# Performance work log

Hardware: AMD Instinct MI355X
Metric: run time of the kernel (lower is better)

## Reference

```python
import jax, jax.numpy as jnp
import numpy as np

N_NODES = 100000
N_EDGES = 600000
IN_FEAT = 128
HID = 128
N_CLASSES = 64


def setup_inputs() -> dict:
    key = jax.random.key(0)
    ks = jax.random.split(key, 24)
    inp = {}
    inp["x"] = jax.random.normal(ks[0], (N_NODES, IN_FEAT), dtype=jnp.float32)
    for i, r in enumerate(["r0", "r1"]):
        inp[f"src_{r}"] = jax.random.randint(ks[1 + 3 * i], (N_EDGES,), 0, N_NODES, dtype=jnp.int32)
        inp[f"dst_{r}"] = jax.random.randint(ks[2 + 3 * i], (N_EDGES,), 0, N_NODES, dtype=jnp.int32)
        inp[f"ew_{r}"] = jax.random.uniform(ks[3 + 3 * i], (N_EDGES,), dtype=jnp.float32)
    def glorot(k, shape):
        fan = (shape[0] + shape[1]) / 2.0
        return jax.random.normal(k, shape, dtype=jnp.float32) / jnp.sqrt(fan)
    j = 7
    for r in ["r0", "r1"]:
        inp[f"Ws0_{r}"] = glorot(ks[j], (IN_FEAT, HID)); j += 1
        inp[f"Wn0_{r}"] = glorot(ks[j], (IN_FEAT, HID)); j += 1
        inp[f"b0_{r}"] = jnp.zeros((HID,), jnp.float32)
        inp[f"Wp_{r}"] = glorot(ks[j], (HID, HID)); j += 1
        inp[f"bp_{r}"] = jnp.zeros((HID,), jnp.float32)
        inp[f"Ws1_{r}"] = glorot(ks[j], (HID, N_CLASSES)); j += 1
        inp[f"Wn1_{r}"] = glorot(ks[j], (HID, N_CLASSES)); j += 1
        inp[f"b1_{r}"] = jnp.zeros((N_CLASSES,), jnp.float32)
    return inp


def _mean_agg(feat, src, dst, ew, n_nodes):
    # edge-weighted messages, mean over in-edges (divide by in-degree as DGL does)
    msg = feat[src] * ew[:, None]                      # [E, d]
    s = jax.ops.segment_sum(msg, dst, num_segments=n_nodes)
    deg = jax.ops.segment_sum(jnp.ones_like(ew), dst, num_segments=n_nodes)
    return s / jnp.maximum(deg, 1.0)[:, None]


def _max_agg(feat, src, dst, ew, n_nodes):
    msg = feat[src] * ew[:, None]                      # [E, d]
    m = jax.ops.segment_max(msg, dst, num_segments=n_nodes)
    deg = jax.ops.segment_sum(jnp.ones_like(ew), dst, num_segments=n_nodes)
    return jnp.where(deg[:, None] > 0, m, 0.0)         # zero for isolated nodes


def reference(x, src_r0, dst_r0, ew_r0, src_r1, dst_r1, ew_r1,
              Ws0_r0, Wn0_r0, b0_r0, Ws0_r1, Wn0_r1, b0_r1,
              Wp_r0, bp_r0, Ws1_r0, Wn1_r0, b1_r0,
              Wp_r1, bp_r1, Ws1_r1, Wn1_r1, b1_r1):
    n = x.shape[0]
    # Layer 0: per-relation SAGEConv(mean), HeteroGraphConv aggregate='sum', then relu
    h = jnp.zeros((n, Wn0_r0.shape[1]), x.dtype)
    for src, dst, ew, Ws, Wn, b in [
        (src_r0, dst_r0, ew_r0, Ws0_r0, Wn0_r0, b0_r0),
        (src_r1, dst_r1, ew_r1, Ws0_r1, Wn0_r1, b0_r1),
    ]:
        agg = _mean_agg(x, src, dst, ew, n)
        h = h + x @ Ws + agg @ Wn + b
    h = jax.nn.relu(h)
    # Classifier layer: per-relation SAGEConv(pool): relu(fc_pool(h_src)) -> max-agg
    logits = jnp.zeros((n, Wn1_r0.shape[1]), x.dtype)
    for src, dst, ew, Wp, bp, Ws, Wn, b in [
        (src_r0, dst_r0, ew_r0, Wp_r0, bp_r0, Ws1_r0, Wn1_r0, b1_r0),
        (src_r1, dst_r1, ew_r1, Wp_r1, bp_r1, Ws1_r1, Wn1_r1, b1_r1),
    ]:
        hp = jax.nn.relu(h @ Wp + bp)
        agg = _max_agg(hp, src, dst, ew, n)
        logits = logits + h @ Ws + agg @ Wn + b
    return logits
```

## Files before the change

### kernel.cpp

```cpp
#include <hip/hip_runtime.h>

typedef short bf16x8 __attribute__((ext_vector_type(8)));
typedef float f32x4 __attribute__((ext_vector_type(4)));
typedef unsigned short u16;
typedef unsigned int u32;

#define NN 100000
#define NE 600000
#define PART 12500
#define ECH 4688

__device__ __forceinline__ u16 f2b(float f) {
    u32 u = __float_as_uint(f);
    return (u16)((u + 0x7FFFu + ((u >> 16) & 1u)) >> 16);
}

__global__ void fused_setup(
    const float* __restrict__ x, u16* __restrict__ xo,
    const float* __restrict__ Ws0_0, const float* __restrict__ Ws0_1,
    const float* __restrict__ Wn0_0, const float* __restrict__ Wn0_1,
    const float* __restrict__ Wp_0,  const float* __restrict__ Wp_1,
    const float* __restrict__ Ws1_0, const float* __restrict__ Ws1_1,
    const float* __restrict__ Wn1_0, const float* __restrict__ Wn1_1,
    const float* __restrict__ b0_0, const float* __restrict__ b0_1,
    const float* __restrict__ b1_0, const float* __restrict__ b1_1,
    const float* __restrict__ bp_0, const float* __restrict__ bp_1,
    u16* __restrict__ w, float* __restrict__ bsum0, float* __restrict__ bsum1,
    float* __restrict__ bpc)
{
    int bb = blockIdx.x;
    if (bb < 12500) {
        int t = bb * 256 + threadIdx.x;
        const float4 v = reinterpret_cast<const float4*>(x)[t];
        ushort4 r; r.x = f2b(v.x); r.y = f2b(v.y); r.z = f2b(v.z); r.w = f2b(v.w);
        reinterpret_cast<ushort4*>(xo)[t] = r;
    } else {
        int t = (bb - 12500) * 256 + threadIdx.x;
        if (t < 81920) {
            int m = t >> 14, u = t & 16383;
            int n = u >> 7, k = u & 127;
            float v;
            if (m == 0)      v = Ws0_0[k * 128 + n] + Ws0_1[k * 128 + n];
            else if (m == 1) v = Wn0_0[k * 128 + n];
            else if (m == 2) v = Wn0_1[k * 128 + n];
            else if (m == 3) v = Wp_0[k * 128 + n];
            else             v = Wp_1[k * 128 + n];
            w[t] = f2b(v);
        } else if (t < 106496) {
            int u = t - 81920;
            int m = u >> 13; u &= 8191;
            int n = u >> 7, k = u & 127;
            float v;
            if (m == 0)      v = Ws1_0[k * 64 + n] + Ws1_1[k * 64 + n];
            else if (m == 1) v = Wn1_0[k * 64 + n];
            else             v = Wn1_1[k * 64 + n];
            w[t] = f2b(v);
        } else if (t < 106624) {
            int i = t - 106496; bsum0[i] = b0_0[i] + b0_1[i];
        } else if (t < 106688) {
            int i = t - 106624; bsum1[i] = b1_0[i] + b1_1[i];
        } else if (t < 106944) {
            int i = t - 106688; bpc[i] = (i < 128) ? bp_0[i] : bp_1[i - 128];
        }
    }
}

__global__ __launch_bounds__(256) void deg_part(
    const int* __restrict__ d0, const int* __restrict__ d1,
    int* __restrict__ g0, int* __restrict__ g1)
{
    int part = blockIdx.x & 7;
    int sub = blockIdx.x >> 3;
    int rel = sub & 1;
    int chunk = sub >> 1;
    const int lo = part * PART, hi = lo + PART;
    const int* d = rel ? d1 : d0;
    int* g = rel ? g1 : g0;
    const int e0 = chunk * ECH;
    const int e1 = min(e0 + ECH, NE);
    for (int e = e0 + threadIdx.x; e < e1; e += 256) {
        int dd = d[e];
        if (dd >= lo && dd < hi) atomicAdd(&g[dd], 1);
    }
}

__global__ void scan_local(const int* __restrict__ deg0, const int* __restrict__ deg1,
                           int* __restrict__ offs0, int* __restrict__ offs1,
                           int* __restrict__ bsA, int* __restrict__ bsB)
{
    __shared__ int sm[1024];
    int rel = blockIdx.x >= 98;
    int blk = blockIdx.x - rel * 98;
    const int* in = rel ? deg1 : deg0;
    int* out = rel ? offs1 : offs0;
    int* bsum = rel ? bsB : bsA;
    int t = threadIdx.x;
    int i = blk * 1024 + t;
    int v = (i < NN) ? in[i] : 0;
    sm[t] = v;
    __syncthreads();
    for (int off = 1; off < 1024; off <<= 1) {
        int add = (t >= off) ? sm[t - off] : 0;
        __syncthreads();
        sm[t] += add;
        __syncthreads();
    }
    if (i < NN) out[i] = sm[t] - v;
    if (t == 1023) bsum[blk] = sm[1023];
}

__global__ void scan_bsums(int* __restrict__ bsA, int* __restrict__ bsB)
{
    __shared__ int sm[128];
    int* bsum = blockIdx.x ? bsB : bsA;
    int t = threadIdx.x;
    int v = (t < 98) ? bsum[t] : 0;
    sm[t] = v;
    __syncthreads();
    for (int off = 1; off < 128; off <<= 1) {
        int add = (t >= off) ? sm[t - off] : 0;
        __syncthreads();
        sm[t] += add;
        __syncthreads();
    }
    if (t < 98) bsum[t] = sm[t] - v;
}

__global__ void scan_add(int* __restrict__ offs0, int* __restrict__ offs1,
                         const int* __restrict__ bsA, const int* __restrict__ bsB,
                         int* __restrict__ cur0, int* __restrict__ cur1,
                         u32* __restrict__ csr0, u32* __restrict__ csr1)
{
    int rel = blockIdx.x >= 392;
    int i = (blockIdx.x - rel * 392) * 256 + threadIdx.x;
    int* offs = rel ? offs1 : offs0;
    int* cur = rel ? cur1 : cur0;
    const int* bsum = rel ? bsB : bsA;
    if (i < NN) {
        int v = offs[i] + bsum[i >> 10];
        offs[i] = v;
        cur[i] = v;
    }
    if (i == 0) offs[NN] = NE;
    if (blockIdx.x == 0 && threadIdx.x < 8) {
        csr0[NE + threadIdx.x] = 0;
        csr1[NE + threadIdx.x] = 0;
    }
}

__global__ __launch_bounds__(256) void build_csr_part(
    const int* __restrict__ src0, const int* __restrict__ dst0,
    const float* __restrict__ ew0,
    const int* __restrict__ src1, const int* __restrict__ dst1,
    const float* __restrict__ ew1,
    int* __restrict__ cur0, int* __restrict__ cur1,
    u32* __restrict__ csr0, u32* __restrict__ csr1)
{
    int part = blockIdx.x & 7;
    int sub = blockIdx.x >> 3;
    int rel = sub & 1;
    int chunk = sub >> 1;
    const int lo = part * PART, hi = lo + PART;
    const int* src = rel ? src1 : src0;
    const int* dst = rel ? dst1 : dst0;
    const float* ew = rel ? ew1 : ew0;
    int* cur = rel ? cur1 : cur0;
    u32* csr = rel ? csr1 : csr0;
    const int e0 = chunk * ECH;
    const int e1 = min(e0 + ECH, NE);
    for (int e = e0 + threadIdx.x; e < e1; e += 256) {
        int d = dst[e];
        if (d >= lo && d < hi) {
            int p = atomicAdd(&cur[d], 1);
            u32 q = (__float_as_uint(ew[e]) + 0x10000u) >> 17;
            csr[p] = ((u32)src[e] << 15) | q;
        }
    }
}

template<bool MAXAGG>
__global__ __launch_bounds__(256) void gather(
    const u16* __restrict__ F0, const u16* __restrict__ F1,
    const int* __restrict__ offs0, const u32* __restrict__ csr0, u16* __restrict__ o0,
    const int* __restrict__ offs1, const u32* __restrict__ csr1, u16* __restrict__ o1)
{
    int b = blockIdx.x;
    int rel = b >= 25000;
    const u16* F = rel ? F1 : F0;
    const int* offs = rel ? offs1 : offs0;
    const u32* csr = rel ? csr1 : csr0;
    u16* out = rel ? o1 : o0;
    int node = (b - rel * 25000) * 4 + (threadIdx.x >> 6);
    int lane = threadIdx.x & 63;
    int beg = __builtin_amdgcn_readfirstlane(offs[node]);
    int end = __builtin_amdgcn_readfirstlane(offs[node + 1]);
    const int lane2 = lane << 1;

    float acc0[8], acc1[8];
#pragma unroll
    for (int i = 0; i < 8; ++i) { acc0[i] = 0.f; acc1[i] = 0.f; }

    for (int e = beg; e < end; e += 8) {
        u32 E[8];
#pragma unroll
        for (int i = 0; i < 8; ++i)
            E[i] = __builtin_amdgcn_readfirstlane(csr[e + i]);
        float wq[8];
        wq[0] = __uint_as_float(E[0] << 17);
#pragma unroll
        for (int i = 1; i < 8; ++i)
            wq[i] = (e + i < end) ? __uint_as_float(E[i] << 17) : 0.f;
        u32 v[8];
#pragma unroll
        for (int i = 0; i < 8; ++i)
            v[i] = *reinterpret_cast<const u32*>(F + ((size_t)(E[i] >> 15) << 7) + lane2);
#pragma unroll
        for (int i = 0; i < 8; ++i) {
            float f0 = __uint_as_float(v[i] << 16);
            float f1 = __uint_as_float(v[i] & 0xFFFF0000u);
            if (MAXAGG) {
                acc0[i] = fmaxf(acc0[i], f0 * wq[i]);
                acc1[i] = fmaxf(acc1[i], f1 * wq[i]);
            } else {
                acc0[i] = fmaf(f0, wq[i], acc0[i]);
                acc1[i] = fmaf(f1, wq[i], acc1[i]);
            }
        }
    }

    float a0, a1, scale;
    if (MAXAGG) {
        a0 = fmaxf(fmaxf(fmaxf(acc0[0], acc0[1]), fmaxf(acc0[2], acc0[3])),
                   fmaxf(fmaxf(acc0[4], acc0[5]), fmaxf(acc0[6], acc0[7])));
        a1 = fmaxf(fmaxf(fmaxf(acc1[0], acc1[1]), fmaxf(acc1[2], acc1[3])),
                   fmaxf(fmaxf(acc1[4], acc1[5]), fmaxf(acc1[6], acc1[7])));
        scale = 1.f;
    } else {
        a0 = ((acc0[0] + acc0[1]) + (acc0[2] + acc0[3])) +
             ((acc0[4] + acc0[5]) + (acc0[6] + acc0[7]));
        a1 = ((acc1[0] + acc1[1]) + (acc1[2] + acc1[3])) +
             ((acc1[4] + acc1[5]) + (acc1[6] + acc1[7]));
        scale = 1.f / fmaxf((float)(end - beg), 1.f);
    }
    ushort2 r; r.x = f2b(a0 * scale); r.y = f2b(a1 * scale);
    *reinterpret_cast<ushort2*>(out + (size_t)node * 128 + lane2) = r;
}

template<int NPAIR, int COLGROUPS, int WAVES, bool RELU, bool OUTF32, bool DUAL>
__global__ __launch_bounds__(WAVES * 64, 2) void gemm_reg(
    const u16* __restrict__ A0, const u16* __restrict__ A1, const u16* __restrict__ A2,
    const u16* __restrict__ BT, const float* __restrict__ bias,
    float* __restrict__ outF, u16* __restrict__ outB, u16* __restrict__ outB2)
{
    constexpr int NC = COLGROUPS * 32;
    constexpr int RT = WAVES / COLGROUPS;
    constexpr int OST = DUAL ? (NC / 2) : NC;
    constexpr int NTILES = NN / 32;
    const int w = threadIdx.x >> 6, l = threadIdx.x & 63;
    const int cg = w % COLGROUPS, rsub = w / COLGROUPS;
    const int l15 = l & 15, lk = (l >> 4) << 3, rq = (l >> 4) << 2;

    bf16x8 bfr[NPAIR][4][2];
#pragma unroll
    for (int p = 0; p < NPAIR; ++p)
#pragma unroll
        for (int ks = 0; ks < 4; ++ks)
#pragma unroll
            for (int cf = 0; cf < 2; ++cf) {
                int n = p * NC + cg * 32 + cf * 16 + l15;
                bfr[p][ks][cf] = *reinterpret_cast<const bf16x8*>(BT + (size_t)n * 128 + ks * 32 + lk);
            }

    const u16* As[3] = {A0, A1, A2};
    const float bv0 = bias[cg * 32 + l15];
    const float bv1 = bias[cg * 32 + 16 + l15];

    for (int tile = blockIdx.x * RT + rsub; tile < NTILES; tile += gridDim.x * RT) {
        const size_t rowbase = (size_t)tile * 32;

        bf16x8 af[NPAIR][4][2];
#pragma unroll
        for (int p = 0; p < NPAIR; ++p) {
            const u16* A = As[p] + rowbase * 128;
#pragma unroll
            for (int ks = 0; ks < 4; ++ks) {
                const int k0 = ks * 32 + lk;
                af[p][ks][0] = *reinterpret_cast<const bf16x8*>(A + (size_t)l15 * 128 + k0);
                af[p][ks][1] = *reinterpret_cast<const bf16x8*>(A + (size_t)(16 + l15) * 128 + k0);
            }
        }

        f32x4 acc[2][2];
#pragma unroll
        for (int rf = 0; rf < 2; ++rf)
#pragma unroll
            for (int cf = 0; cf < 2; ++cf)
                acc[rf][cf] = f32x4{0.f, 0.f, 0.f, 0.f};

#pragma unroll
        for (int p = 0; p < NPAIR; ++p)
#pragma unroll
            for (int ks = 0; ks < 4; ++ks) {
                acc[0][0] = __builtin_amdgcn_mfma_f32_16x16x32_bf16(af[p][ks][0], bfr[p][ks][0], acc[0][0], 0, 0, 0);
                acc[0][1] = __builtin_amdgcn_mfma_f32_16x16x32_bf16(af[p][ks][0], bfr[p][ks][1], acc[0][1], 0, 0, 0);
                acc[1][0] = __builtin_amdgcn_mfma_f32_16x16x32_bf16(af[p][ks][1], bfr[p][ks][0], acc[1][0], 0, 0, 0);
                acc[1][1] = __builtin_amdgcn_mfma_f32_16x16x32_bf16(af[p][ks][1], bfr[p][ks][1], acc[1][1], 0, 0, 0);
            }

        u16* ob = outB;
        if (DUAL && cg >= 4) ob = outB2;
        const int colbase = (DUAL ? (cg & 3) : cg) * 32;
#pragma unroll
        for (int cf = 0; cf < 2; ++cf) {
            const int col = colbase + cf * 16 + l15;
            const float bv = cf ? bv1 : bv0;
#pragma unroll
            for (int rf = 0; rf < 2; ++rf) {
#pragma unroll
                for (int j = 0; j < 4; ++j) {
                    const size_t row = rowbase + rf * 16 + rq + j;
                    float v = acc[rf][cf][j] + bv;
                    if (RELU) v = fmaxf(v, 0.f);
                    if (OUTF32) outF[row * OST + col] = v;
                    else        ob[row * OST + col] = f2b(v);
                }
            }
        }
    }
}

extern "C" void kernel_launch(void* const* d_in, const int* in_sizes, int n_in,
                              void* d_out, int out_size, void* d_ws, size_t ws_size,
                              hipStream_t stream)
{
    const float* x     = (const float*)d_in[0];
    const int*   src0  = (const int*)d_in[1];
    const int*   dst0  = (const int*)d_in[2];
    const float* ew0   = (const float*)d_in[3];
    const int*   src1  = (const int*)d_in[4];
    const int*   dst1  = (const int*)d_in[5];
    const float* ew1   = (const float*)d_in[6];
    const float* Ws0_0 = (const float*)d_in[7];
    const float* Wn0_0 = (const float*)d_in[8];
    const float* b0_0  = (const float*)d_in[9];
    const float* Wp_0  = (const float*)d_in[10];
    const float* bp_0  = (const float*)d_in[11];
    const float* Ws1_0 = (const float*)d_in[12];
    const float* Wn1_0 = (const float*)d_in[13];
    const float* b1_0  = (const float*)d_in[14];
    const float* Ws0_1 = (const float*)d_in[15];
    const float* Wn0_1 = (const float*)d_in[16];
    const float* b0_1  = (const float*)d_in[17];
    const float* Wp_1  = (const float*)d_in[18];
    const float* bp_1  = (const float*)d_in[19];
    const float* Ws1_1 = (const float*)d_in[20];
    const float* Wn1_1 = (const float*)d_in[21];
    const float* b1_1  = (const float*)d_in[22];

    char* ws = (char*)d_ws;
    u16*   x16   = (u16*)(ws + 0);
    u16*   h16   = (u16*)(ws + 25600000);
    u16*   a0    = (u16*)(ws + 51200000);
    u16*   a1    = (u16*)(ws + 76800000);
    u16*   hp1   = (u16*)(ws + 102400000);
    u32*   csr0  = (u32*)(ws + 128000000);
    u32*   csr1  = (u32*)(ws + 130400032);
    int*   offs0 = (int*)(ws + 132800064);
    int*   offs1 = (int*)(ws + 133200080);
    int*   cur0  = (int*)(ws + 133600096);
    int*   cur1  = (int*)(ws + 134000096);
    int*   deg0  = (int*)(ws + 134400096);
    int*   deg1  = (int*)(ws + 134800096);
    int*   bsA   = (int*)(ws + 135200096);
    int*   bsB   = (int*)(ws + 135200608);
    u16*   wts   = (u16*)(ws + 135201120);
    float* bsum0 = (float*)(ws + 135414112);
    float* bsum1 = (float*)(ws + 135414624);
    float* bpc   = (float*)(ws + 135415136);

    u16* hp0 = x16;

    hipMemsetAsync(deg0, 0, 800000, stream);
    deg_part<<<2048, 256, 0, stream>>>(dst0, dst1, deg0, deg1);
    fused_setup<<<12918, 256, 0, stream>>>(
        x, x16, Ws0_0, Ws0_1, Wn0_0, Wn0_1, Wp_0, Wp_1,
        Ws1_0, Ws1_1, Wn1_0, Wn1_1, b0_0, b0_1, b1_0, b1_1, bp_0, bp_1,
        wts, bsum0, bsum1, bpc);

    scan_local<<<196, 1024, 0, stream>>>(deg0, deg1, offs0, offs1, bsA, bsB);
    scan_bsums<<<2, 128, 0, stream>>>(bsA, bsB);
    scan_add<<<784, 256, 0, stream>>>(offs0, offs1, bsA, bsB, cur0, cur1, csr0, csr1);
    build_csr_part<<<2048, 256, 0, stream>>>(
        src0, dst0, ew0, src1, dst1, ew1, cur0, cur1, csr0, csr1);

    gather<false><<<50000, 256, 0, stream>>>(x16, x16, offs0, csr0, a0, offs1, csr1, a1);
    gemm_reg<3, 4, 4, true, false, false><<<1024, 256, 0, stream>>>(
        x16, a0, a1, wts, bsum0, nullptr, h16, nullptr);

    gemm_reg<1, 8, 8, true, false, true><<<512, 512, 0, stream>>>(
        h16, nullptr, nullptr, wts + 49152, bpc, nullptr, hp0, hp1);
    gather<true><<<50000, 256, 0, stream>>>(hp0, hp1, offs0, csr0, a0, offs1, csr1, a1);
    gemm_reg<3, 2, 4, false, true, false><<<782, 256, 0, stream>>>(
        h16, a0, a1, wts + 81920, bsum1, (float*)d_out, nullptr, nullptr);
}
```

Baseline: 375.4 us.

## Store node features in 16-column slices so gather blocks hit cache-resident partitions

New measurement: 422.5 us. 1.13x slower.

```diff
diff --git a/kernel.cpp b/kernel.cpp
--- a/kernel.cpp
+++ b/kernel.cpp
@@ -9,6 +9,7 @@
 #define NE 600000
 #define PART 12500
 #define ECH 4688
+#define SL (NN * 16)
 
 __device__ __forceinline__ u16 f2b(float f) {
     u32 u = __float_as_uint(f);
@@ -33,7 +34,9 @@
         int t = bb * 256 + threadIdx.x;
         const float4 v = reinterpret_cast<const float4*>(x)[t];
         ushort4 r; r.x = f2b(v.x); r.y = f2b(v.y); r.z = f2b(v.z); r.w = f2b(v.w);
-        reinterpret_cast<ushort4*>(xo)[t] = r;
+        int node = t >> 5;
+        int fq = (t & 31) << 2;
+        *reinterpret_cast<ushort4*>(xo + (size_t)(fq >> 4) * SL + node * 16 + (fq & 15)) = r;
     } else {
         int t = (bb - 12500) * 256 + threadIdx.x;
         if (t < 81920) {
@@ -128,8 +131,7 @@
 
 __global__ void scan_add(int* __restrict__ offs0, int* __restrict__ offs1,
                          const int* __restrict__ bsA, const int* __restrict__ bsB,
-                         int* __restrict__ cur0, int* __restrict__ cur1,
-                         u32* __restrict__ csr0, u32* __restrict__ csr1)
+                         int* __restrict__ cur0, int* __restrict__ cur1)
 {
     int rel = blockIdx.x >= 392;
     int i = (blockIdx.x - rel * 392) * 256 + threadIdx.x;
@@ -142,10 +144,6 @@
         cur[i] = v;
     }
     if (i == 0) offs[NN] = NE;
-    if (blockIdx.x == 0 && threadIdx.x < 8) {
-        csr0[NE + threadIdx.x] = 0;
-        csr1[NE + threadIdx.x] = 0;
-    }
 }
 
 __global__ __launch_bounds__(256) void build_csr_part(
@@ -178,75 +176,73 @@
     }
 }
 
-template<bool MAXAGG>
-__global__ __launch_bounds__(256) void gather(
-    const u16* __restrict__ F0, const u16* __restrict__ F1,
+template<bool MAXAGG, bool REL2>
+__global__ __launch_bounds__(256) void gather_slice(
+    const u16* __restrict__ Fs,
     const int* __restrict__ offs0, const u32* __restrict__ csr0, u16* __restrict__ o0,
     const int* __restrict__ offs1, const u32* __restrict__ csr1, u16* __restrict__ o1)
 {
-    int b = blockIdx.x;
-    int rel = b >= 25000;
-    const u16* F = rel ? F1 : F0;
-    const int* offs = rel ? offs1 : offs0;
-    const u32* csr = rel ? csr1 : csr0;
-    u16* out = rel ? o1 : o0;
-    int node = (b - rel * 25000) * 4 + (threadIdx.x >> 6);
-    int lane = threadIdx.x & 63;
-    int beg = __builtin_amdgcn_readfirstlane(offs[node]);
-    int end = __builtin_amdgcn_readfirstlane(offs[node + 1]);
-    const int lane2 = lane << 1;
-
-    float acc0[8], acc1[8];
-#pragma unroll
-    for (int i = 0; i < 8; ++i) { acc0[i] = 0.f; acc1[i] = 0.f; }
-
-    for (int e = beg; e < end; e += 8) {
-        u32 E[8];
-#pragma unroll
-        for (int i = 0; i < 8; ++i)
-            E[i] = __builtin_amdgcn_readfirstlane(csr[e + i]);
-        float wq[8];
-        wq[0] = __uint_as_float(E[0] << 17);
-#pragma unroll
-        for (int i = 1; i < 8; ++i)
-            wq[i] = (e + i < end) ? __uint_as_float(E[i] << 17) : 0.f;
-        u32 v[8];
-#pragma unroll
-        for (int i = 0; i < 8; ++i)
-            v[i] = *reinterpret_cast<const u32*>(F + ((size_t)(E[i] >> 15) << 7) + lane2);
-#pragma unroll
-        for (int i = 0; i < 8; ++i) {
-            float f0 = __uint_as_float(v[i] << 16);
-            float f1 = __uint_as_float(v[i] & 0xFFFF0000u);
-            if (MAXAGG) {
-                acc0[i] = fmaxf(acc0[i], f0 * wq[i]);
-                acc1[i] = fmaxf(acc1[i], f1 * wq[i]);
-            } else {
-                acc0[i] = fmaf(f0, wq[i], acc0[i]);
-                acc1[i] = fmaf(f1, wq[i], acc1[i]);
+    const int part = blockIdx.x & 7;
+    int sub = blockIdx.x >> 3;
+    const int* offs = offs0;
+    const u32* csr = csr0;
+    u16* outs = o0;
+    int nper;
+    if (REL2) {
+        int rel = sub & 1; sub >>= 1;
+        if (rel) { offs = offs1; csr = csr1; outs = o1; }
+        nper = 782;
+    } else {
+        nper = 391;
+    }
+    const int l = threadIdx.x & 63;
+    const int wv = threadIdx.x >> 6;
+    const int g = l >> 3, lf = l & 7;
+    const u16* F = Fs + (size_t)part * SL + (lf << 1);
+    u16* out = outs + (size_t)part * SL + (lf << 1);
+
+    const int nbeg = sub * nper;
+    const int nend = min(nbeg + nper, NN);
+    for (int nb = nbeg + (wv << 3); nb < nend; nb += 32) {
+        int node = nb + g;
+        int nc = min(node, NN - 1);
+        int beg = offs[nc];
+        int cnt = (node < nend) ? (offs[nc + 1] - beg) : 0;
+        int last = max(cnt - 1, 0);
+        float a0 = 0.f, a1 = 0.f;
+        for (int base = 0; __any(base < cnt); base += 8) {
+            u32 E[8];
+#pragma unroll
+            for (int j = 0; j < 8; ++j)
+                E[j] = csr[beg + min(base + j, last)];
+            u32 v[8];
+#pragma unroll
+            for (int j = 0; j < 8; ++j)
+                v[j] = *reinterpret_cast<const u32*>(F + ((size_t)(E[j] >> 15) << 4));
+#pragma unroll
+            for (int j = 0; j < 8; ++j) {
+                float wgt = (base + j < cnt) ? __uint_as_float(E[j] << 17) : 0.f;
+                float f0 = __uint_as_float(v[j] << 16);
+                float f1 = __uint_as_float(v[j] & 0xFFFF0000u);
+                if (MAXAGG) {
+                    a0 = fmaxf(a0, f0 * wgt);
+                    a1 = fmaxf(a1, f1 * wgt);
+                } else {
+                    a0 = fmaf(f0, wgt, a0);
+                    a1 = fmaf(f1, wgt, a1);
+                }
             }
         }
-    }
-
-    float a0, a1, scale;
-    if (MAXAGG) {
-        a0 = fmaxf(fmaxf(fmaxf(acc0[0], acc0[1]), fmaxf(acc0[2], acc0[3])),
-                   fmaxf(fmaxf(acc0[4], acc0[5]), fmaxf(acc0[6], acc0[7])));
-        a1 = fmaxf(fmaxf(fmaxf(acc1[0], acc1[1]), fmaxf(acc1[2], acc1[3])),
-                   fmaxf(fmaxf(acc1[4], acc1[5]), fmaxf(acc1[6], acc1[7])));
-        scale = 1.f;
-    } else {
-        a0 = ((acc0[0] + acc0[1]) + (acc0[2] + acc0[3])) +
-             ((acc0[4] + acc0[5]) + (acc0[6] + acc0[7]));
-        a1 = ((acc1[0] + acc1[1]) + (acc1[2] + acc1[3])) +
-             ((acc1[4] + acc1[5]) + (acc1[6] + acc1[7]));
-        scale = 1.f / fmaxf((float)(end - beg), 1.f);
-    }
-    ushort2 r; r.x = f2b(a0 * scale); r.y = f2b(a1 * scale);
-    *reinterpret_cast<ushort2*>(out + (size_t)node * 128 + lane2) = r;
-}
-
-template<int NPAIR, int COLGROUPS, int WAVES, bool RELU, bool OUTF32, bool DUAL>
+        if (node < nend) {
+            float s = MAXAGG ? 1.f : 1.f / fmaxf((float)cnt, 1.f);
+            ushort2 r; r.x = f2b(a0 * s); r.y = f2b(a1 * s);
+            *reinterpret_cast<ushort2*>(out + (size_t)node * 16) = r;
+        }
+    }
+}
+
+template<int NPAIR, int COLGROUPS, int WAVES, bool RELU, bool OUTF32, bool DUAL,
+         int SLICEMASK, bool SLICEC>
 __global__ __launch_bounds__(WAVES * 64, 2) void gemm_reg(
     const u16* __restrict__ A0, const u16* __restrict__ A1, const u16* __restrict__ A2,
     const u16* __restrict__ BT, const float* __restrict__ bias,
@@ -281,12 +277,21 @@
         bf16x8 af[NPAIR][4][2];
 #pragma unroll
         for (int p = 0; p < NPAIR; ++p) {
-            const u16* A = As[p] + rowbase * 128;
+            const u16* A = As[p];
+            const bool sl = (SLICEMASK >> p) & 1;
 #pragma unroll
             for (int ks = 0; ks < 4; ++ks) {
                 const int k0 = ks * 32 + lk;
-                af[p][ks][0] = *reinterpret_cast<const bf16x8*>(A + (size_t)l15 * 128 + k0);
-                af[p][ks][1] = *reinterpret_cast<const bf16x8*>(A + (size_t)(16 + l15) * 128 + k0);
+                size_t off0, off1;
+                if (sl) {
+                    off0 = (size_t)(k0 >> 4) * SL + (rowbase + l15) * 16 + (k0 & 15);
+                    off1 = (size_t)(k0 >> 4) * SL + (rowbase + 16 + l15) * 16 + (k0 & 15);
+                } else {
+                    off0 = (rowbase + l15) * (size_t)128 + k0;
+                    off1 = (rowbase + 16 + l15) * (size_t)128 + k0;
+                }
+                af[p][ks][0] = *reinterpret_cast<const bf16x8*>(A + off0);
+                af[p][ks][1] = *reinterpret_cast<const bf16x8*>(A + off1);
             }
         }
 
@@ -314,6 +319,7 @@
         for (int cf = 0; cf < 2; ++cf) {
             const int col = colbase + cf * 16 + l15;
             const float bv = cf ? bv1 : bv0;
+            const size_t sbase = (size_t)((colbase + cf * 16) >> 4) * SL;
 #pragma unroll
             for (int rf = 0; rf < 2; ++rf) {
 #pragma unroll
@@ -321,8 +327,9 @@
                     const size_t row = rowbase + rf * 16 + rq + j;
                     float v = acc[rf][cf][j] + bv;
                     if (RELU) v = fmaxf(v, 0.f);
-                    if (OUTF32) outF[row * OST + col] = v;
-                    else        ob[row * OST + col] = f2b(v);
+                    if (OUTF32)      outF[row * OST + col] = v;
+                    else if (SLICEC) ob[sbase + row * 16 + l15] = f2b(v);
+                    else             ob[row * OST + col] = f2b(v);
                 }
             }
         }
@@ -358,11 +365,11 @@
     const float* b1_1  = (const float*)d_in[22];
 
     char* ws = (char*)d_ws;
-    u16*   x16   = (u16*)(ws + 0);
+    u16*   x16s  = (u16*)(ws + 0);
     u16*   h16   = (u16*)(ws + 25600000);
-    u16*   a0    = (u16*)(ws + 51200000);
-    u16*   a1    = (u16*)(ws + 76800000);
-    u16*   hp1   = (u16*)(ws + 102400000);
+    u16*   a0s   = (u16*)(ws + 51200000);
+    u16*   a1s   = (u16*)(ws + 76800000);
+    u16*   hp1s  = (u16*)(ws + 102400000);
     u32*   csr0  = (u32*)(ws + 128000000);
     u32*   csr1  = (u32*)(ws + 130400032);
     int*   offs0 = (int*)(ws + 132800064);
@@ -378,28 +385,32 @@
     float* bsum1 = (float*)(ws + 135414624);
     float* bpc   = (float*)(ws + 135415136);
 
-    u16* hp0 = x16;
+    u16* hp0s = x16s;
 
     hipMemsetAsync(deg0, 0, 800000, stream);
     deg_part<<<2048, 256, 0, stream>>>(dst0, dst1, deg0, deg1);
     fused_setup<<<12918, 256, 0, stream>>>(
-        x, x16, Ws0_0, Ws0_1, Wn0_0, Wn0_1, Wp_0, Wp_1,
+        x, x16s, Ws0_0, Ws0_1, Wn0_0, Wn0_1, Wp_0, Wp_1,
         Ws1_0, Ws1_1, Wn1_0, Wn1_1, b0_0, b0_1, b1_0, b1_1, bp_0, bp_1,
         wts, bsum0, bsum1, bpc);
 
     scan_local<<<196, 1024, 0, stream>>>(deg0, deg1, offs0, offs1, bsA, bsB);
     scan_bsums<<<2, 128, 0, stream>>>(bsA, bsB);
-    scan_add<<<784, 256, 0, stream>>>(offs0, offs1, bsA, bsB, cur0, cur1, csr0, csr1);
+    scan_add<<<784, 256, 0, stream>>>(offs0, offs1, bsA, bsB, cur0, cur1);
     build_csr_part<<<2048, 256, 0, stream>>>(
         src0, dst0, ew0, src1, dst1, ew1, cur0, cur1, csr0, csr1);
 
-    gather<false><<<50000, 256, 0, stream>>>(x16, x16, offs0, csr0, a0, offs1, csr1, a1);
-    gemm_reg<3, 4, 4, true, false, false><<<1024, 256, 0, stream>>>(
-        x16, a0, a1, wts, bsum0, nullptr, h16, nullptr);
-
-    gemm_reg<1, 8, 8, true, false, true><<<512, 512, 0, stream>>>(
-        h16, nullptr, nullptr, wts + 49152, bpc, nullptr, hp0, hp1);
-    gather<true><<<50000, 256, 0, stream>>>(hp0, hp1, offs0, csr0, a0, offs1, csr1, a1);
-    gemm_reg<3, 2, 4, false, true, false><<<782, 256, 0, stream>>>(
-        h16, a0, a1, wts + 81920, bsum1, (float*)d_out, nullptr, nullptr);
-}
+    gather_slice<false, true><<<2048, 256, 0, stream>>>(
+        x16s, offs0, csr0, a0s, offs1, csr1, a1s);
+    gemm_reg<3, 4, 4, true, false, false, 0b111, false><<<1024, 256, 0, stream>>>(
+        x16s, a0s, a1s, wts, bsum0, nullptr, h16, nullptr);
+
+    gemm_reg<1, 8, 8, true, false, true, 0, true><<<512, 512, 0, stream>>>(
+        h16, nullptr, nullptr, wts + 49152, bpc, nullptr, hp0s, hp1s);
+    gather_slice<true, false><<<2048, 256, 0, stream>>>(
+        hp0s, offs0, csr0, a0s, nullptr, nullptr, nullptr);
+    gather_slice<true, false><<<2048, 256, 0, stream>>>(
+        hp1s, offs1, csr1, a1s, nullptr, nullptr, nullptr);
+    gemm_reg<3, 2, 4, false, true, false, 0b110, false><<<782, 256, 0, stream>>>(
+        h16, a0s, a1s, wts + 81920, bsum1, (float*)d_out, nullptr, nullptr);
+}
```

## Fuse layer-0 mean gather into GEMM via LDS and merge degree count into setup

Applied to the files above, without the earlier changes.

Measured after the change: 372.4 us. No clear change (-0.8%).

```diff
diff --git a/kernel.cpp b/kernel.cpp
--- a/kernel.cpp
+++ b/kernel.cpp
@@ -26,16 +26,32 @@
     const float* __restrict__ b1_0, const float* __restrict__ b1_1,
     const float* __restrict__ bp_0, const float* __restrict__ bp_1,
     u16* __restrict__ w, float* __restrict__ bsum0, float* __restrict__ bsum1,
-    float* __restrict__ bpc)
+    float* __restrict__ bpc,
+    const int* __restrict__ d0, const int* __restrict__ d1,
+    int* __restrict__ g0, int* __restrict__ g1)
 {
     int bb = blockIdx.x;
-    if (bb < 12500) {
-        int t = bb * 256 + threadIdx.x;
+    if (bb < 2048) {
+        int part = bb & 7;
+        int sub = bb >> 3;
+        int rel = sub & 1;
+        int chunk = sub >> 1;
+        const int lo = part * PART, hi = lo + PART;
+        const int* d = rel ? d1 : d0;
+        int* g = rel ? g1 : g0;
+        const int e0 = chunk * ECH;
+        const int e1 = min(e0 + ECH, NE);
+        for (int e = e0 + threadIdx.x; e < e1; e += 256) {
+            int dd = d[e];
+            if (dd >= lo && dd < hi) atomicAdd(&g[dd], 1);
+        }
+    } else if (bb < 14548) {
+        int t = (bb - 2048) * 256 + threadIdx.x;
         const float4 v = reinterpret_cast<const float4*>(x)[t];
         ushort4 r; r.x = f2b(v.x); r.y = f2b(v.y); r.z = f2b(v.z); r.w = f2b(v.w);
         reinterpret_cast<ushort4*>(xo)[t] = r;
     } else {
-        int t = (bb - 12500) * 256 + threadIdx.x;
+        int t = (bb - 14548) * 256 + threadIdx.x;
         if (t < 81920) {
             int m = t >> 14, u = t & 16383;
             int n = u >> 7, k = u & 127;
@@ -65,25 +81,6 @@
     }
 }
 
-__global__ __launch_bounds__(256) void deg_part(
-    const int* __restrict__ d0, const int* __restrict__ d1,
-    int* __restrict__ g0, int* __restrict__ g1)
-{
-    int part = blockIdx.x & 7;
-    int sub = blockIdx.x >> 3;
-    int rel = sub & 1;
-    int chunk = sub >> 1;
-    const int lo = part * PART, hi = lo + PART;
-    const int* d = rel ? d1 : d0;
-    int* g = rel ? g1 : g0;
-    const int e0 = chunk * ECH;
-    const int e1 = min(e0 + ECH, NE);
-    for (int e = e0 + threadIdx.x; e < e1; e += 256) {
-        int dd = d[e];
-        if (dd >= lo && dd < hi) atomicAdd(&g[dd], 1);
-    }
-}
-
 __global__ void scan_local(const int* __restrict__ deg0, const int* __restrict__ deg1,
                            int* __restrict__ offs0, int* __restrict__ offs1,
                            int* __restrict__ bsA, int* __restrict__ bsB)
@@ -178,8 +175,7 @@
     }
 }
 
-template<bool MAXAGG>
-__global__ __launch_bounds__(256) void gather(
+__global__ __launch_bounds__(256) void gather_max(
     const u16* __restrict__ F0, const u16* __restrict__ F1,
     const int* __restrict__ offs0, const u32* __restrict__ csr0, u16* __restrict__ o0,
     const int* __restrict__ offs1, const u32* __restrict__ csr1, u16* __restrict__ o1)
@@ -191,59 +187,129 @@
     const u32* csr = rel ? csr1 : csr0;
     u16* out = rel ? o1 : o0;
     int node = (b - rel * 25000) * 4 + (threadIdx.x >> 6);
-    int lane = threadIdx.x & 63;
+    int lane2 = (threadIdx.x & 63) << 1;
     int beg = __builtin_amdgcn_readfirstlane(offs[node]);
     int end = __builtin_amdgcn_readfirstlane(offs[node + 1]);
-    const int lane2 = lane << 1;
-
-    float acc0[8], acc1[8];
-#pragma unroll
-    for (int i = 0; i < 8; ++i) { acc0[i] = 0.f; acc1[i] = 0.f; }
-
+
+    float a0 = 0.f, a1 = 0.f;
     for (int e = beg; e < end; e += 8) {
-        u32 E[8];
+        u32 E[8], v[8];
 #pragma unroll
         for (int i = 0; i < 8; ++i)
-            E[i] = __builtin_amdgcn_readfirstlane(csr[e + i]);
-        float wq[8];
-        wq[0] = __uint_as_float(E[0] << 17);
-#pragma unroll
-        for (int i = 1; i < 8; ++i)
-            wq[i] = (e + i < end) ? __uint_as_float(E[i] << 17) : 0.f;
-        u32 v[8];
+            E[i] = csr[e + i];
 #pragma unroll
         for (int i = 0; i < 8; ++i)
             v[i] = *reinterpret_cast<const u32*>(F + ((size_t)(E[i] >> 15) << 7) + lane2);
 #pragma unroll
         for (int i = 0; i < 8; ++i) {
-            float f0 = __uint_as_float(v[i] << 16);
-            float f1 = __uint_as_float(v[i] & 0xFFFF0000u);
-            if (MAXAGG) {
-                acc0[i] = fmaxf(acc0[i], f0 * wq[i]);
-                acc1[i] = fmaxf(acc1[i], f1 * wq[i]);
-            } else {
-                acc0[i] = fmaf(f0, wq[i], acc0[i]);
-                acc1[i] = fmaf(f1, wq[i], acc1[i]);
-            }
-        }
-    }
-
-    float a0, a1, scale;
-    if (MAXAGG) {
-        a0 = fmaxf(fmaxf(fmaxf(acc0[0], acc0[1]), fmaxf(acc0[2], acc0[3])),
-                   fmaxf(fmaxf(acc0[4], acc0[5]), fmaxf(acc0[6], acc0[7])));
-        a1 = fmaxf(fmaxf(fmaxf(acc1[0], acc1[1]), fmaxf(acc1[2], acc1[3])),
-                   fmaxf(fmaxf(acc1[4], acc1[5]), fmaxf(acc1[6], acc1[7])));
-        scale = 1.f;
-    } else {
-        a0 = ((acc0[0] + acc0[1]) + (acc0[2] + acc0[3])) +
-             ((acc0[4] + acc0[5]) + (acc0[6] + acc0[7]));
-        a1 = ((acc1[0] + acc1[1]) + (acc1[2] + acc1[3])) +
-             ((acc1[4] + acc1[5]) + (acc1[6] + acc1[7]));
-        scale = 1.f / fmaxf((float)(end - beg), 1.f);
-    }
-    ushort2 r; r.x = f2b(a0 * scale); r.y = f2b(a1 * scale);
+            float wgt = (e + i < end) ? __uint_as_float(E[i] << 17) : 0.f;
+            a0 = fmaxf(a0, __uint_as_float(v[i] << 16) * wgt);
+            a1 = fmaxf(a1, __uint_as_float(v[i] & 0xFFFF0000u) * wgt);
+        }
+    }
+    ushort2 r; r.x = f2b(a0); r.y = f2b(a1);
     *reinterpret_cast<ushort2*>(out + (size_t)node * 128 + lane2) = r;
+}
+
+__global__ __launch_bounds__(512) void fused_l0(
+    const u16* __restrict__ x16,
+    const int* __restrict__ offs0, const u32* __restrict__ csr0,
+    const int* __restrict__ offs1, const u32* __restrict__ csr1,
+    const u16* __restrict__ BT, const float* __restrict__ bias,
+    u16* __restrict__ outB)
+{
+    __shared__ char lds[64 * 256];
+    const int tile = blockIdx.x;
+    const int wv = threadIdx.x >> 6;
+    const int l = threadIdx.x & 63;
+    const int lane2 = l << 1;
+
+    for (int j = 0; j < 4; ++j) {
+        const int nl = (wv << 2) + j;
+        const int node = tile * 32 + nl;
+        int begA = offs0[node], cntA = offs0[node + 1] - begA;
+        int begB = offs1[node], cntB = offs1[node + 1] - begB;
+        int lastA = max(cntA - 1, 0), lastB = max(cntB - 1, 0);
+        float a0A = 0.f, a1A = 0.f, a0B = 0.f, a1B = 0.f;
+        const int mx = max(cntA, cntB);
+        for (int base = 0; base < mx; base += 8) {
+            u32 EA[8], EB[8], vA[8], vB[8];
+#pragma unroll
+            for (int q = 0; q < 8; ++q) {
+                EA[q] = csr0[begA + min(base + q, lastA)];
+                EB[q] = csr1[begB + min(base + q, lastB)];
+            }
+#pragma unroll
+            for (int q = 0; q < 8; ++q) {
+                vA[q] = *reinterpret_cast<const u32*>(x16 + ((size_t)(EA[q] >> 15) << 7) + lane2);
+                vB[q] = *reinterpret_cast<const u32*>(x16 + ((size_t)(EB[q] >> 15) << 7) + lane2);
+            }
+#pragma unroll
+            for (int q = 0; q < 8; ++q) {
+                float wA = (base + q < cntA) ? __uint_as_float(EA[q] << 17) : 0.f;
+                float wB = (base + q < cntB) ? __uint_as_float(EB[q] << 17) : 0.f;
+                a0A = fmaf(__uint_as_float(vA[q] << 16), wA, a0A);
+                a1A = fmaf(__uint_as_float(vA[q] & 0xFFFF0000u), wA, a1A);
+                a0B = fmaf(__uint_as_float(vB[q] << 16), wB, a0B);
+                a1B = fmaf(__uint_as_float(vB[q] & 0xFFFF0000u), wB, a1B);
+            }
+        }
+        float sA = 1.f / fmaxf((float)cntA, 1.f);
+        float sB = 1.f / fmaxf((float)cntB, 1.f);
+        const int rowA = nl, rowB = 32 + nl;
+        *reinterpret_cast<u32*>(&lds[(rowA * 256 + l * 4) ^ ((rowA & 7) << 4)]) =
+            (u32)f2b(a0A * sA) | ((u32)f2b(a1A * sA) << 16);
+        *reinterpret_cast<u32*>(&lds[(rowB * 256 + l * 4) ^ ((rowB & 7) << 4)]) =
+            (u32)f2b(a0B * sB) | ((u32)f2b(a1B * sB) << 16);
+    }
+    __syncthreads();
+
+    const int l15 = l & 15, lk = (l >> 4) << 3, rq = (l >> 4) << 2;
+    bf16x8 bfr[3][4];
+#pragma unroll
+    for (int p = 0; p < 3; ++p)
+#pragma unroll
+        for (int ks = 0; ks < 4; ++ks) {
+            int n = p * 128 + wv * 16 + l15;
+            bfr[p][ks] = *reinterpret_cast<const bf16x8*>(BT + (size_t)n * 128 + ks * 32 + lk);
+        }
+    const size_t rowbase = (size_t)tile * 32;
+    bf16x8 a0f[4], a1f[4];
+#pragma unroll
+    for (int ks = 0; ks < 4; ++ks) {
+        int k0 = ks * 32 + lk;
+        a0f[ks] = *reinterpret_cast<const bf16x8*>(x16 + (rowbase + l15) * 128 + k0);
+        a1f[ks] = *reinterpret_cast<const bf16x8*>(x16 + (rowbase + 16 + l15) * 128 + k0);
+    }
+    f32x4 acc0 = f32x4{0.f, 0.f, 0.f, 0.f};
+    f32x4 acc1 = f32x4{0.f, 0.f, 0.f, 0.f};
+#pragma unroll
+    for (int ks = 0; ks < 4; ++ks) {
+        acc0 = __builtin_amdgcn_mfma_f32_16x16x32_bf16(a0f[ks], bfr[0][ks], acc0, 0, 0, 0);
+        acc1 = __builtin_amdgcn_mfma_f32_16x16x32_bf16(a1f[ks], bfr[0][ks], acc1, 0, 0, 0);
+    }
+#pragma unroll
+    for (int p = 1; p < 3; ++p) {
+        const int rbase = (p - 1) * 32;
+#pragma unroll
+        for (int ks = 0; ks < 4; ++ks) {
+            int k0 = ks * 32 + lk;
+            int row0 = rbase + l15, row1 = rbase + 16 + l15;
+            bf16x8 fa0 = *reinterpret_cast<const bf16x8*>(
+                &lds[(row0 * 256 + k0 * 2) ^ ((row0 & 7) << 4)]);
+            bf16x8 fa1 = *reinterpret_cast<const bf16x8*>(
+                &lds[(row1 * 256 + k0 * 2) ^ ((row1 & 7) << 4)]);
+            acc0 = __builtin_amdgcn_mfma_f32_16x16x32_bf16(fa0, bfr[p][ks], acc0, 0, 0, 0);
+            acc1 = __builtin_amdgcn_mfma_f32_16x16x32_bf16(fa1, bfr[p][ks], acc1, 0, 0, 0);
+        }
+    }
+    const int col = wv * 16 + l15;
+    const float bv = bias[col];
+#pragma unroll
+    for (int j = 0; j < 4; ++j) {
+        outB[(rowbase + rq + j) * 128 + col] = f2b(fmaxf(acc0[j] + bv, 0.f));
+        outB[(rowbase + 16 + rq + j) * 128 + col] = f2b(fmaxf(acc1[j] + bv, 0.f));
+    }
 }
 
 template<int NPAIR, int COLGROUPS, int WAVES, bool RELU, bool OUTF32, bool DUAL>
@@ -381,11 +447,10 @@
     u16* hp0 = x16;
 
     hipMemsetAsync(deg0, 0, 800000, stream);
-    deg_part<<<2048, 256, 0, stream>>>(dst0, dst1, deg0, deg1);
-    fused_setup<<<12918, 256, 0, stream>>>(
+    fused_setup<<<14966, 256, 0, stream>>>(
         x, x16, Ws0_0, Ws0_1, Wn0_0, Wn0_1, Wp_0, Wp_1,
         Ws1_0, Ws1_1, Wn1_0, Wn1_1, b0_0, b0_1, b1_0, b1_1, bp_0, bp_1,
-        wts, bsum0, bsum1, bpc);
+        wts, bsum0, bsum1, bpc, dst0, dst1, deg0, deg1);
 
     scan_local<<<196, 1024, 0, stream>>>(deg0, deg1, offs0, offs1, bsA, bsB);
     scan_bsums<<<2, 128, 0, stream>>>(bsA, bsB);
@@ -393,13 +458,13 @@
     build_csr_part<<<2048, 256, 0, stream>>>(
         src0, dst0, ew0, src1, dst1, ew1, cur0, cur1, csr0, csr1);
 
-    gather<false><<<50000, 256, 0, stream>>>(x16, x16, offs0, csr0, a0, offs1, csr1, a1);
-    gemm_reg<3, 4, 4, true, false, false><<<1024, 256, 0, stream>>>(
-        x16, a0, a1, wts, bsum0, nullptr, h16, nullptr);
+    fused_l0<<<3125, 512, 0, stream>>>(
+        x16, offs0, csr0, offs1, csr1, wts, bsum0, h16);
 
     gemm_reg<1, 8, 8, true, false, true><<<512, 512, 0, stream>>>(
         h16, nullptr, nullptr, wts + 49152, bpc, nullptr, hp0, hp1);
-    gather<true><<<50000, 256, 0, stream>>>(hp0, hp1, offs0, csr0, a0, offs1, csr1, a1);
+    gather_max<<<50000, 256, 0, stream>>>(
+        hp0, hp1, offs0, csr0, a0, offs1, csr1, a1);
     gemm_reg<3, 2, 4, false, true, false><<<782, 256, 0, stream>>>(
         h16, a0, a1, wts + 81920, bsum1, (float*)d_out, nullptr, nullptr);
 }
```
